# Performance work log

Measured on AMD Instinct MI355X. Metric: run time of the kernel, lower is better.

The kernel has to match this reference:

```python
import jax, jax.numpy as jnp
import numpy as np

T = 32            # num_tsteps
B = 8192          # batch_size
W_IN0, W_OUT0 = 36, 18
W_IN1, W_OUT1 = 18, 8
TILE0, TILE1 = 2, 1
BETA = (0.95, 0.95)
TH = (0.55, 0.25)
Q = 15000.0       # sephia mrr_Q
ER_DB = 20.0      # sephia extinction ratio
IL_DB = 0.0       # sephia insertion loss
SHIFT_PM = -250.0 # sephia resonance shift per unit spike
P_UNITY = 1e-4    # dbm_to_watt(-10): optical power per WDM channel at unit input


def _lif(inp, mem, beta, th):
    # snntorch Leaky, reset_mechanism='zero', reset_delay=True:
    # reset decided from incoming mem, membrane zeroed before leak+integrate.
    reset = (mem > th).astype(inp.dtype)
    mem_new = (beta * mem + inp) * (1.0 - reset)
    spk = (mem_new > th).astype(inp.dtype)
    return spk, mem_new


def _allpass(spk, wl_nm):
    # All-pass MRR modulator: spike shifts the ring resonance by SHIFT_PM.
    # Normalized detuning delta = shift / (FWHM/2), FWHM = lambda / Q.
    fwhm_pm = wl_nm * 1e3 / Q                      # [C]
    delta = (spk * SHIFT_PM) / (0.5 * fwhm_pm)     # [B, C]
    gamma = 10.0 ** (-ER_DB / 20.0)                # on-resonance amplitude (ER)
    il = 10.0 ** (-IL_DB / 20.0)                   # insertion loss factor
    return (il * (1j * delta + gamma) / (1j * delta + 1.0)).astype(jnp.complex64)


def setup_inputs() -> dict:
    key = jax.random.key(0)
    ks = jax.random.split(key, 6)
    return {
        "x_in": jax.random.uniform(ks[0], (T, B, W_IN0), jnp.float32),
        "W0": jax.random.uniform(ks[1], (TILE0, W_IN0 // TILE0, W_OUT0 * 2 // TILE0), jnp.float32),
        "d0": jax.random.normal(ks[2], (TILE0, W_OUT0 // TILE0), jnp.float32) * 5e3,
        "W1": jax.random.uniform(ks[3], (TILE1, W_IN1 // TILE1, W_OUT1 * 2 // TILE1), jnp.float32),
        "d1": jax.random.normal(ks[4], (TILE1, W_OUT1 // TILE1), jnp.float32) * 5e3,
        "peak_powers_dbm": jax.random.uniform(ks[5], (W_IN0,), jnp.float32, -15.0, -5.0),
    }


def reference(x_in, W0, d0, W1, d1, peak_powers_dbm):
    wl0 = 1550.0 + 0.8 * jnp.arange(W_OUT0, dtype=jnp.float32)   # MRR resonance wavelengths (nm)
    # sephia_inputs: sqrt(dbm_to_watt(P_dbm) * 1e6) field amplitude per channel
    amp0 = jnp.sqrt((10.0 ** (peak_powers_dbm[:W_OUT0] / 10.0) / 1000.0) * 1e6)
    S0 = W_OUT0 * 2 // TILE0   # 18 spatial channels after EO broadcast
    S1 = W_OUT1 * 2 // TILE1   # 16 spatial channels into layer 1

    def step(carry, x_t):
        mem0, mem1 = carry
        b = x_t.shape[0]
        # --- EO conversion + layer 0 MRR weight bank (power domain) ---
        p_in = x_t * P_UNITY                                     # [B, 36] optical power
        p0 = jnp.broadcast_to(p_in[:, :, None], (b, W_IN0, S0)).reshape(b, TILE0, W_IN0 // TILE0, S0)
        I0 = jnp.einsum('btws,tws->bts', p0, W0)                 # photocurrents [B,2,18]
        cur0 = ((I0[..., 0::2] - I0[..., 1::2]) * d0).reshape(b, W_OUT0)  # balanced PDs + Diagonal
        spk0, mem0 = _lif(cur0, mem0, BETA[0], TH[0])
        # --- SEPhIA all-pass MRR modulation of comb lines ---
        lo = _allpass(spk0, wl0) * amp0.astype(jnp.complex64)    # [B, 18] complex field
        pw0 = jnp.abs(lo) ** 2                                   # detected power == spike record
        # --- post-SEPhIA broadcast + layer 1 weight bank ---
        p1 = jnp.broadcast_to(pw0[:, :, None], (b, W_IN1, S1)).reshape(b, TILE1, W_IN1 // TILE1, S1)
        I1 = jnp.einsum('btws,tws->bts', p1, W1)                 # [B,1,16]
        cur1 = ((I1[..., 0::2] - I1[..., 1::2]) * d1).reshape(b, W_OUT1)
        spk1, mem1 = _lif(cur1, mem1, BETA[1], TH[1])
        return (mem0, mem1), (pw0, spk1, mem0, mem1)

    mem0 = jnp.zeros((x_in.shape[1], W_OUT0), x_in.dtype)
    mem1 = jnp.zeros((x_in.shape[1], W_OUT1), x_in.dtype)
    _, (spks0, spks1, mems0, mems1) = jax.lax.scan(step, (mem0, mem1), x_in)
    return spks0, spks1, mems0, mems1
```

## Files before the change

kernel.cpp:

```cpp
#include <hip/hip_runtime.h>


namespace {
constexpr int Tn = 32;
constexpr int Bn = 8192;
constexpr unsigned O_PW = 0;
constexpr unsigned O_S1 = Tn * Bn * 18;
constexpr unsigned O_M0 = O_S1 + Tn * Bn * 8;
constexpr unsigned O_M1 = O_M0 + Tn * Bn * 18;
}

template <int IMM>
__device__ __forceinline__ float swzf(float v) {
    return __int_as_float(__builtin_amdgcn_ds_swizzle(__float_as_int(v), IMM));
}

__global__ __launch_bounds__(256, 4)
void oesnn_kernel(const float* __restrict__ x_in,
                  const float* __restrict__ W0g,
                  const float* __restrict__ d0g,
                  const float* __restrict__ W1g,
                  const float* __restrict__ d1g,
                  const float* __restrict__ peakg,
                  float* __restrict__ out)
{
    const int wv   = threadIdx.x >> 6;
    const int lane = threadIdx.x & 63;
    const int half = lane >> 5;
    const int l5   = lane & 31;
    const int b    = blockIdx.x * 8 + wv * 2 + half;

    const int  c    = (l5 < 18) ? l5 : 17;
    const int  tl   = c / 9;
    const int  jc   = c - 9 * tl;
    const int  col  = l5 & 15;
    const int  o1   = col >> 1;
    const bool isL0  = l5 < 18;
    const bool isOut1 = (l5 < 16) && !(l5 & 1);

    float w0e[18], w0o[18];
    #pragma unroll
    for (int w = 0; w < 18; ++w) {
        const float2 p = *(const float2*)(W0g + (tl * 18 + w) * 18 + 2 * jc);
        w0e[w] = p.x;
        w0o[w] = p.y;
    }
    float w1[18];
    #pragma unroll
    for (int w = 0; w < 18; ++w)
        w1[w] = W1g[w * 16 + col];

    const float dd0 = d0g[c];
    const float dd1 = d1g[o1];

    float pon, poff;
    {
        const float wl    = 1550.0f + 0.8f * (float)c;
        const float halfw = 0.5f * (wl * 1e3f / 15000.0f);
        const float amp   = sqrtf((exp10f(peakg[c] / 10.0f) / 1000.0f) * 1e6f);
        const float lr0   = 0.1f * amp;
        const float a0    = sqrtf(lr0 * lr0);
        poff = a0 * a0;
        const float delta = -250.0f / halfw;
        const float den   = fmaf(delta, delta, 1.0f);
        const float qr    = fmaf(delta, delta, 0.1f) / den;
        const float qi    = (delta - 0.1f * delta) / den;
        const float lr = qr * amp, li = qi * amp;
        const float a  = sqrtf(fmaf(lr, lr, li * li));
        pon = a * a;
    }

    float mem0 = 0.f, mem1 = 0.f;
    unsigned xoff  = (unsigned)b * 36 + (unsigned)tl * 18;
    unsigned opw_i = O_PW + (unsigned)b * 18 + (unsigned)c;
    unsigned om0_i = O_M0 + (unsigned)b * 18 + (unsigned)c;
    unsigned os1_i = O_S1 + (unsigned)b * 8 + (unsigned)o1;
    unsigned om1_i = O_M1 + (unsigned)b * 8 + (unsigned)o1;

    float2 xv[9];
    {
        const float2* xp2 = (const float2*)(x_in + xoff);
        #pragma unroll
        for (int k = 0; k < 9; ++k) xv[k] = xp2[k];
    }

    #pragma unroll 2
    for (int t = 0; t < Tn; ++t) {
        float se = 0.f, so = 0.f;
        #pragma unroll
        for (int k = 0; k < 9; ++k) {
            const float p0 = xv[k].x * 1e-4f;
            const float p1 = xv[k].y * 1e-4f;
            se = fmaf(p0, w0e[2 * k],     se);
            so = fmaf(p0, w0o[2 * k],     so);
            se = fmaf(p1, w0e[2 * k + 1], se);
            so = fmaf(p1, w0o[2 * k + 1], so);
        }

        xoff += Bn * 36;
        if (t < Tn - 1) {
            const float2* xp2 = (const float2*)(x_in + xoff);
            #pragma unroll
            for (int k = 0; k < 9; ++k) xv[k] = xp2[k];
        }

        const float c0  = (se - so) * dd0;
        const float m2A = (mem0 > 0.55f) ? 0.0f : fmaf(0.95f, mem0, c0);
        mem0 = m2A;
        const float pw  = (m2A > 0.55f) ? pon : poff;

        if (isL0) {
            out[opw_i] = pw;
            out[om0_i] = m2A;
        }

        float pwall[18];
        #define GATHER(k) pwall[k] = swzf<((k) << 5)>(pw);
        GATHER(0)  GATHER(1)  GATHER(2)  GATHER(3)  GATHER(4)  GATHER(5)
        GATHER(6)  GATHER(7)  GATHER(8)  GATHER(9)  GATHER(10) GATHER(11)
        GATHER(12) GATHER(13) GATHER(14) GATHER(15) GATHER(16) GATHER(17)
        #undef GATHER

        float i1 = 0.f;
        #pragma unroll
        for (int w = 0; w < 18; ++w)
            i1 = fmaf(pwall[w], w1[w], i1);

        const float i1p = swzf<0x041F>(i1);
        const float c1  = (i1 - i1p) * dd1;
        const float m2B = (mem1 > 0.25f) ? 0.0f : fmaf(0.95f, mem1, c1);
        mem1 = m2B;

        if (isOut1) {
            out[os1_i] = (m2B > 0.25f) ? 1.0f : 0.0f;
            out[om1_i] = m2B;
        }

        opw_i += Bn * 18;
        om0_i += Bn * 18;
        os1_i += Bn * 8;
        om1_i += Bn * 8;
    }
}

extern "C" void kernel_launch(void* const* d_in, const int* in_sizes, int n_in,
                              void* d_out, int out_size, void* d_ws, size_t ws_size,
                              hipStream_t stream) {
    (void)in_sizes; (void)n_in; (void)out_size; (void)d_ws; (void)ws_size;
    const float* x  = (const float*)d_in[0];
    const float* W0 = (const float*)d_in[1];
    const float* d0 = (const float*)d_in[2];
    const float* W1 = (const float*)d_in[3];
    const float* d1 = (const float*)d_in[4];
    const float* pk = (const float*)d_in[5];
    float* out = (float*)d_out;

    dim3 grid(Bn / 8), block(256);
    hipLaunchKernelGGL(oesnn_kernel, grid, block, 0, stream,
                       x, W0, d0, W1, d1, pk, out);
}
```

Baseline: 127.3 us.

## Replace swizzle gather with spike ballot and precomputed layer-1 deltas

```diff
diff --git a/kernel.cpp b/kernel.cpp
--- a/kernel.cpp
+++ b/kernel.cpp
@@ -10,9 +10,21 @@
 constexpr unsigned O_M1 = O_M0 + Tn * Bn * 18;
 }
 
-template <int IMM>
-__device__ __forceinline__ float swzf(float v) {
-    return __int_as_float(__builtin_amdgcn_ds_swizzle(__float_as_int(v), IMM));
+__device__ __forceinline__ void sephia_pw(int c, const float* peakg,
+                                          float& pon, float& poff) {
+    const float wl    = 1550.0f + 0.8f * (float)c;
+    const float halfw = 0.5f * (wl * 1e3f / 15000.0f);
+    const float amp   = sqrtf((exp10f(peakg[c] / 10.0f) / 1000.0f) * 1e6f);
+    const float lr0   = 0.1f * amp;
+    const float a0    = sqrtf(lr0 * lr0);
+    poff = a0 * a0;
+    const float delta = -250.0f / halfw;
+    const float den   = fmaf(delta, delta, 1.0f);
+    const float qr    = fmaf(delta, delta, 0.1f) / den;
+    const float qi    = (delta - 0.1f * delta) / den;
+    const float lr = qr * amp, li = qi * amp;
+    const float a  = sqrtf(fmaf(lr, lr, li * li));
+    pon = a * a;
 }
 
 __global__ __launch_bounds__(256, 4)
@@ -30,13 +42,12 @@
     const int l5   = lane & 31;
     const int b    = blockIdx.x * 8 + wv * 2 + half;
 
-    const int  c    = (l5 < 18) ? l5 : 17;
-    const int  tl   = c / 9;
-    const int  jc   = c - 9 * tl;
-    const int  col  = l5 & 15;
-    const int  o1   = col >> 1;
-    const bool isL0  = l5 < 18;
-    const bool isOut1 = (l5 < 16) && !(l5 & 1);
+    const int  c  = (l5 < 18) ? l5 : 17;
+    const int  tl = c / 9;
+    const int  jc = c - 9 * tl;
+    const int  o  = (l5 >= 18 && l5 < 26) ? (l5 - 18) : 0;
+    const bool isL0   = l5 < 18;
+    const bool isOut1 = (l5 >= 18) && (l5 < 26);
 
     float w0e[18], w0o[18];
     #pragma unroll
@@ -45,37 +56,40 @@
         w0e[w] = p.x;
         w0o[w] = p.y;
     }
-    float w1[18];
+    float dd0 = d0g[c];
+    float pon, poff;
+    sephia_pw(c, peakg, pon, poff);
+
+    float dd1 = d1g[o];
+    float base1, d1c[18];
+    {
+        float se_b = 0.f, so_b = 0.f;
+        #pragma unroll
+        for (int c2 = 0; c2 < 18; ++c2) {
+            float pon2, poff2;
+            sephia_pw(c2, peakg, pon2, poff2);
+            const float w1e = W1g[c2 * 16 + 2 * o];
+            const float w1o = W1g[c2 * 16 + 2 * o + 1];
+            se_b = fmaf(poff2, w1e, se_b);
+            so_b = fmaf(poff2, w1o, so_b);
+            d1c[c2] = (pon2 - poff2) * (w1e - w1o) * dd1;
+        }
+        base1 = (se_b - so_b) * dd1;
+    }
+
     #pragma unroll
-    for (int w = 0; w < 18; ++w)
-        w1[w] = W1g[w * 16 + col];
-
-    const float dd0 = d0g[c];
-    const float dd1 = d1g[o1];
-
-    float pon, poff;
-    {
-        const float wl    = 1550.0f + 0.8f * (float)c;
-        const float halfw = 0.5f * (wl * 1e3f / 15000.0f);
-        const float amp   = sqrtf((exp10f(peakg[c] / 10.0f) / 1000.0f) * 1e6f);
-        const float lr0   = 0.1f * amp;
-        const float a0    = sqrtf(lr0 * lr0);
-        poff = a0 * a0;
-        const float delta = -250.0f / halfw;
-        const float den   = fmaf(delta, delta, 1.0f);
-        const float qr    = fmaf(delta, delta, 0.1f) / den;
-        const float qi    = (delta - 0.1f * delta) / den;
-        const float lr = qr * amp, li = qi * amp;
-        const float a  = sqrtf(fmaf(lr, lr, li * li));
-        pon = a * a;
+    for (int i = 0; i < 18; ++i) {
+        asm volatile("" : "+v"(w0e[i]), "+v"(w0o[i]), "+v"(d1c[i]));
     }
+    asm volatile("" : "+v"(dd0), "+v"(pon), "+v"(poff));
+    asm volatile("" : "+v"(base1), "+v"(dd1));
 
     float mem0 = 0.f, mem1 = 0.f;
     unsigned xoff  = (unsigned)b * 36 + (unsigned)tl * 18;
     unsigned opw_i = O_PW + (unsigned)b * 18 + (unsigned)c;
     unsigned om0_i = O_M0 + (unsigned)b * 18 + (unsigned)c;
-    unsigned os1_i = O_S1 + (unsigned)b * 8 + (unsigned)o1;
-    unsigned om1_i = O_M1 + (unsigned)b * 8 + (unsigned)o1;
+    unsigned os1_i = O_S1 + (unsigned)b * 8 + (unsigned)o;
+    unsigned om1_i = O_M1 + (unsigned)b * 8 + (unsigned)o;
 
     float2 xv[9];
     {
@@ -83,6 +97,8 @@
         #pragma unroll
         for (int k = 0; k < 9; ++k) xv[k] = xp2[k];
     }
+
+    const int shift = half * 32;
 
     #pragma unroll 2
     for (int t = 0; t < Tn; ++t) {
@@ -114,21 +130,17 @@
             out[om0_i] = m2A;
         }
 
-        float pwall[18];
-        #define GATHER(k) pwall[k] = swzf<((k) << 5)>(pw);
-        GATHER(0)  GATHER(1)  GATHER(2)  GATHER(3)  GATHER(4)  GATHER(5)
-        GATHER(6)  GATHER(7)  GATHER(8)  GATHER(9)  GATHER(10) GATHER(11)
-        GATHER(12) GATHER(13) GATHER(14) GATHER(15) GATHER(16) GATHER(17)
-        #undef GATHER
+        const unsigned long long bal = __ballot(m2A > 0.55f);
+        const unsigned grp = (unsigned)(bal >> shift);
 
-        float i1 = 0.f;
+        float cur = base1;
         #pragma unroll
-        for (int w = 0; w < 18; ++w)
-            i1 = fmaf(pwall[w], w1[w], i1);
+        for (int c2 = 0; c2 < 18; ++c2) {
+            const float s = (float)((grp >> c2) & 1u);
+            cur = fmaf(s, d1c[c2], cur);
+        }
 
-        const float i1p = swzf<0x041F>(i1);
-        const float c1  = (i1 - i1p) * dd1;
-        const float m2B = (mem1 > 0.25f) ? 0.0f : fmaf(0.95f, mem1, c1);
+        const float m2B = (mem1 > 0.25f) ? 0.0f : fmaf(0.95f, mem1, cur);
         mem1 = m2B;
 
         if (isOut1) {
```

Result: slower. 135.1 us (+6.1%).
